# Kernel optimization log

Hardware: AMD Instinct MI355X
Metric: run time of the kernel (lower is better)

The kernel has to match this reference:

```python
import jax, jax.numpy as jnp
import numpy as np

B, S, D = 8, 1024, 576
H, HD = 9, 64
LAT = 144
FF = 1536
N_ROUTED, TOP_K = 7, 2
EPS = 1e-5
THETA = 10000.0


def setup_inputs() -> dict:
    key = jax.random.key(0)
    ks = jax.random.split(key, 20)
    sc = lambda fan_in: 1.0 / np.sqrt(fan_in)
    inp = {
        "x": jax.random.normal(ks[0], (B, S, D), jnp.float32),
        "ln1_w": jnp.ones((D,), jnp.float32),
        "ln2_w": jnp.ones((D,), jnp.float32),
        # attention projections, torch Linear layout (out, in)
        "Wqd": jax.random.normal(ks[1], (LAT, D), jnp.float32) * sc(D),
        "Wkvd": jax.random.normal(ks[2], (LAT, D), jnp.float32) * sc(D),
        "Wqu": jax.random.normal(ks[3], (D, LAT), jnp.float32) * sc(LAT),
        "Wku": jax.random.normal(ks[4], (D, LAT), jnp.float32) * sc(LAT),
        "Wvu": jax.random.normal(ks[5], (D, LAT), jnp.float32) * sc(LAT),
        "Wo": jax.random.normal(ks[6], (D, D), jnp.float32) * sc(D),
        # shared expert SwiGLU
        "sg": jax.random.normal(ks[7], (FF, D), jnp.float32) * sc(D),
        "su": jax.random.normal(ks[8], (FF, D), jnp.float32) * sc(D),
        "sd": jax.random.normal(ks[9], (D, FF), jnp.float32) * sc(FF),
        # routed experts, stacked [E, out, in]
        "rg": jax.random.normal(ks[10], (N_ROUTED, FF, D), jnp.float32) * sc(D),
        "ru": jax.random.normal(ks[11], (N_ROUTED, FF, D), jnp.float32) * sc(D),
        "rd": jax.random.normal(ks[12], (N_ROUTED, D, FF), jnp.float32) * sc(FF),
        "Wr": jax.random.normal(ks[13], (N_ROUTED, D), jnp.float32) * sc(D),
        "rb": jnp.zeros((N_ROUTED,), jnp.float32),
    }
    return inp


def _rmsnorm(x, w, eps=EPS):
    xf = x.astype(jnp.float32)
    y = xf * jax.lax.rsqrt(jnp.mean(xf * xf, axis=-1, keepdims=True) + eps)
    return y.astype(x.dtype) * w


def _rotate_half(x):
    x1, x2 = x[..., : x.shape[-1] // 2], x[..., x.shape[-1] // 2 :]
    return jnp.concatenate((-x2, x1), axis=-1)


def _rope(q, k, seq_len):
    inv_freq = 1.0 / THETA ** (jnp.arange(0, HD, 2, dtype=jnp.float32) / HD)
    freqs = jnp.arange(seq_len, dtype=jnp.float32)[:, None] * inv_freq  # [S, HD/2]
    emb = jnp.concatenate((freqs, freqs), axis=-1)  # [S, HD]
    cos = jnp.cos(emb)[None, None, :, :]
    sin = jnp.sin(emb)[None, None, :, :]
    return q * cos + _rotate_half(q) * sin, k * cos + _rotate_half(k) * sin


def _swiglu(h, Wg, Wu, Wd):
    return (jax.nn.silu(h @ Wg.T) * (h @ Wu.T)) @ Wd.T


def reference(x, ln1_w, ln2_w, Wqd, Wkvd, Wqu, Wku, Wvu, Wo,
              sg, su, sd, rg, ru, rd, Wr, rb):
    bsz, seq_len, _ = x.shape
    # ---- attention sublayer ----
    residual = x
    h = _rmsnorm(x, ln1_w)
    q_lat = h @ Wqd.T
    kv_lat = h @ Wkvd.T
    q = (q_lat @ Wqu.T).reshape(bsz, seq_len, H, HD).transpose(0, 2, 1, 3)
    k = (kv_lat @ Wku.T).reshape(bsz, seq_len, H, HD).transpose(0, 2, 1, 3)
    v = (kv_lat @ Wvu.T).reshape(bsz, seq_len, H, HD).transpose(0, 2, 1, 3)
    q, k = _rope(q, k, seq_len)
    scores = jnp.einsum("bhqd,bhkd->bhqk", q, k) / jnp.sqrt(jnp.float32(HD))
    causal = jnp.tril(jnp.ones((seq_len, seq_len), bool))
    scores = jnp.where(causal, scores, jnp.float32(-jnp.inf))
    attn = jax.nn.softmax(scores, axis=-1)
    o = jnp.einsum("bhqk,bhkd->bhqd", attn, v).transpose(0, 2, 1, 3).reshape(bsz, seq_len, D)
    x = residual + o @ Wo.T
    # ---- MoE sublayer ----
    residual = x
    h = _rmsnorm(x, ln2_w)
    shared = _swiglu(h, sg, su, sd)  # 1 shared expert
    logits = h @ Wr.T + rb
    probs = jax.nn.sigmoid(logits)
    scores_k, idx = jax.lax.top_k(probs, TOP_K)  # [B,S,K]
    scores_k = scores_k / jnp.sum(scores_k, axis=-1, keepdims=True)
    # per-token weight for each routed expert [B,S,E]
    w = jnp.sum(jax.nn.one_hot(idx, N_ROUTED, dtype=h.dtype) * scores_k[..., None], axis=-2)
    combined = jnp.zeros_like(h)
    for e in range(N_ROUTED):  # small fixed expert count
        combined = combined + w[..., e : e + 1] * _swiglu(h, rg[e], ru[e], rd[e])
    return residual + shared + combined
```

## Files before the change

kernel.cpp:

```cpp
#include <hip/hip_runtime.h>
#include <stdint.h>
#include <math.h>

#define B_    8
#define S_    1024
#define D_    576
#define H_    9
#define HD_   64
#define LAT_  144
#define FF_   1536
#define NE_   7
#define NT_   8192
#define NPAIR_ 16384
#define NACT_  24576
#define MAXT_ 200

typedef unsigned short u16;
typedef __attribute__((ext_vector_type(8))) short bf16x8;
typedef __attribute__((ext_vector_type(4))) float f32x4;
typedef __attribute__((ext_vector_type(4))) unsigned short us4;

__device__ __forceinline__ u16 f2b(float f){
  union{float f;uint32_t u;} v; v.f=f;
  uint32_t u=v.u;
  return (u16)((u + 0x7fffu + ((u>>16)&1u))>>16);
}
__device__ __forceinline__ float b2f(u16 h){
  union{uint32_t u;float f;} v; v.u=((uint32_t)h)<<16; return v.f;
}

#define MFMA16(a,b,c) __builtin_amdgcn_mfma_f32_16x16x32_bf16((a),(b),(c),0,0,0)

typedef __attribute__((address_space(1))) const unsigned char g_u8;
typedef __attribute__((address_space(3))) unsigned char s_u8;
__device__ __forceinline__ void gll16(const void* g, void* l){
  __builtin_amdgcn_global_load_lds((g_u8*)g, (s_u8*)l, 16, 0, 0);
}

struct CvtSegs {
  const float* src[6];
  u16* dst[6];
  int start4[7];
};
__global__ void k_cvt(CvtSegs cs){
  int tot = cs.start4[6];
  for(int i = blockIdx.x*blockDim.x + threadIdx.x; i < tot; i += gridDim.x*blockDim.x){
    int s=0;
    #pragma unroll
    for(int j=0;j<6;j++) if(i >= cs.start4[j+1]) s=j+1;
    int loc = i - cs.start4[s];
    float4 v = ((const float4*)cs.src[s])[loc];
    us4 o; o[0]=f2b(v.x); o[1]=f2b(v.y); o[2]=f2b(v.z); o[3]=f2b(v.w);
    ((us4*)cs.dst[s])[loc] = o;
  }
}

struct CvtSegs2 {
  const float* src[3];
  u16* dhi[3]; u16* dlo[3];
  int start4[4];
};
__global__ void k_cvt_split(CvtSegs2 cs){
  int tot = cs.start4[3];
  for(int i = blockIdx.x*blockDim.x + threadIdx.x; i < tot; i += gridDim.x*blockDim.x){
    int s=0;
    #pragma unroll
    for(int j=0;j<3;j++) if(i >= cs.start4[j+1]) s=j+1;
    int loc = i - cs.start4[s];
    float4 v = ((const float4*)cs.src[s])[loc];
    us4 oh, ol;
    float vv[4]={v.x,v.y,v.z,v.w};
    #pragma unroll
    for(int j=0;j<4;j++){ u16 hh=f2b(vv[j]); oh[j]=hh; ol[j]=f2b(vv[j]-b2f(hh)); }
    ((us4*)cs.dhi[s])[loc]=oh;
    ((us4*)cs.dlo[s])[loc]=ol;
  }
}

__global__ void k_cvt_pad_split(const float* __restrict__ Wqu, const float* __restrict__ Wku,
                                const float* __restrict__ Wvu,
                                u16* __restrict__ dhi, u16* __restrict__ dlo){
  int i = blockIdx.x*256 + threadIdx.x;
  if(i >= 3*D_*160) return;
  int z = i/(D_*160); int rem = i - z*D_*160;
  int row = rem/160, col = rem - row*160;
  const float* s = (z==0)?Wqu:((z==1)?Wku:Wvu);
  float v = (col<LAT_)? s[row*LAT_+col] : 0.f;
  u16 hh=f2b(v);
  dhi[i]=hh; dlo[i]=f2b(v-b2f(hh));
}

__global__ void k_rope_tab(float* __restrict__ cost, float* __restrict__ sint){
  int i = blockIdx.x*256+threadIdx.x; if(i>=S_*32) return;
  int s=i>>5, d=i&31;
  float pw = (float)pow(10000.0, (double)d/32.0);
  float inv = 1.0f/pw;
  float ang = (float)s*inv;
  cost[i]=cosf(ang); sint[i]=sinf(ang);
}

__global__ __launch_bounds__(64) void k_rms(const float* __restrict__ x, const float* __restrict__ w,
                      u16* __restrict__ hhi, u16* __restrict__ hlo){
  int t = blockIdx.x; int lane = threadIdx.x;
  const float* xr = x + (size_t)t*D_;
  float v[9]; float ss=0.f;
  #pragma unroll
  for(int j=0;j<9;j++){ v[j]=xr[lane+64*j]; ss += v[j]*v[j]; }
  #pragma unroll
  for(int m=1;m<64;m<<=1) ss += __shfl_xor(ss,m,64);
  float sc = 1.0f/sqrtf(ss/(float)D_ + 1e-5f);
  #pragma unroll
  for(int j=0;j<9;j++){
    float y = v[j]*sc*w[lane+64*j];
    size_t o=(size_t)t*D_+lane+64*j;
    u16 hh=f2b(y); hhi[o]=hh; hlo[o]=f2b(y-b2f(hh));
  }
}

__global__ __launch_bounds__(256) void k_rms_router(const float* __restrict__ x2, const float* __restrict__ w,
                        const float* __restrict__ Wr, const float* __restrict__ rb,
                        u16* __restrict__ hb, int* __restrict__ idx2, float* __restrict__ w2){
  int wid=threadIdx.x>>6, lane=threadIdx.x&63;
  int t = blockIdx.x*4 + wid;
  const float* xr = x2 + (size_t)t*D_;
  float v[9]; float ss=0.f;
  #pragma unroll
  for(int j=0;j<9;j++){ v[j]=xr[lane+64*j]; ss += v[j]*v[j]; }
  #pragma unroll
  for(int m=1;m<64;m<<=1) ss += __shfl_xor(ss,m,64);
  float sc = 1.0f/sqrtf(ss/(float)D_ + 1e-5f);
  float hv[9];
  #pragma unroll
  for(int j=0;j<9;j++){
    float y = v[j]*sc*w[lane+64*j];
    hv[j]=y;
    hb[(size_t)t*D_+lane+64*j]=f2b(y);
  }
  float pr[7];
  #pragma unroll
  for(int e=0;e<7;e++){
    float s=0.f;
    #pragma unroll
    for(int j=0;j<9;j++) s += hv[j]*Wr[e*D_+lane+64*j];
    #pragma unroll
    for(int mm=1;mm<64;mm<<=1) s+=__shfl_xor(s,mm,64);
    pr[e] = 1.f/(1.f+expf(-(s+rb[e])));
  }
  int e0=0; float b0=pr[0];
  #pragma unroll
  for(int e=1;e<7;e++) if(pr[e]>b0){b0=pr[e];e0=e;}
  int e1=-1; float b1=-1e30f;
  #pragma unroll
  for(int e=0;e<7;e++) if(e!=e0 && pr[e]>b1){b1=pr[e];e1=e;}
  if(lane==0){
    float s=b0+b1;
    idx2[2*t]=e0; idx2[2*t+1]=e1;
    w2[2*t]=b0/s; w2[2*t+1]=b1/s;
  }
}

template<int EPI>
__global__ __launch_bounds__(256) void k_gemm2(
    const u16* __restrict__ Ahi, const u16* __restrict__ Alo, int lda, int aofs_z,
    const u16* __restrict__ Bhi, const u16* __restrict__ Blo, int ldb, long bStrideZ,
    int N, int ksteps,
    u16* __restrict__ Chi, u16* __restrict__ Clo, int ldc,
    float* __restrict__ C32, long cStrideZ, const float* __restrict__ resid)
{
  __shared__ u16 Ahs[128*32], Als[128*32], Bhs[128*32], Bls[128*32];
  int tid=threadIdx.x, wid=tid>>6, lane=tid&63;
  int m0=blockIdx.x*128, n0=blockIdx.y*128, z=blockIdx.z;
  const u16* Abh = Ahi + ((z>0)?aofs_z:0);
  const u16* Abl = Alo + ((z>0)?aofs_z:0);
  const u16* Bbh = Bhi + (long)z*bStrideZ;
  const u16* Bbl = Blo + (long)z*bStrideZ;
  int lq=lane&15, lg=lane>>4;
  int wr=wid>>1, wc=wid&1;
  f32x4 acc[4][4]={};
  for(int kt=0;kt<ksteps;kt++){
    #pragma unroll
    for(int is=0;is<2;is++){
      int ub = is*4096 + wid*1024;
      int o = ub + lane*16;
      int row = o>>6, p=(o>>4)&3;
      int sc8 = ((p ^ ((row>>1)&3)))*8;
      long aoff = (long)(m0+row)*lda + kt*32 + sc8;
      gll16(Abh+aoff, (char*)Ahs+ub);
      gll16(Abl+aoff, (char*)Als+ub);
      int rowb = n0+row; rowb = rowb<N?rowb:(N-1);
      long boff = (long)rowb*ldb + kt*32 + sc8;
      gll16(Bbh+boff, (char*)Bhs+ub);
      gll16(Bbl+boff, (char*)Bls+ub);
    }
    __syncthreads();
    bf16x8 ah[4], al[4], bh[4], bl[4];
    #pragma unroll
    for(int m=0;m<4;m++){
      int arow=wr*64+m*16+lq;
      int co = arow*32 + ((lg ^ ((arow>>1)&3)))*8;
      ah[m]=*(const bf16x8*)&Ahs[co];
      al[m]=*(const bf16x8*)&Als[co];
    }
    #pragma unroll
    for(int n=0;n<4;n++){
      int brow=wc*64+n*16+lq;
      int co = brow*32 + ((lg ^ ((brow>>1)&3)))*8;
      bh[n]=*(const bf16x8*)&Bhs[co];
      bl[n]=*(const bf16x8*)&Bls[co];
    }
    #pragma unroll
    for(int m=0;m<4;m++)
      #pragma unroll
      for(int n=0;n<4;n++){
        acc[m][n]=MFMA16(ah[m],bh[n],acc[m][n]);
        acc[m][n]=MFMA16(ah[m],bl[n],acc[m][n]);
        acc[m][n]=MFMA16(al[m],bh[n],acc[m][n]);
      }
    __syncthreads();
  }
  #pragma unroll
  for(int m=0;m<4;m++){
    #pragma unroll
    for(int n=0;n<4;n++){
      int col = n0 + wc*64 + n*16 + lq;
      if(col<N){
        #pragma unroll
        for(int r=0;r<4;r++){
          int row = m0 + wr*64 + m*16 + lg*4 + r;
          float val = acc[m][n][r];
          if(EPI==0){
            int dc = (col<144)? col : col+16;
            u16 hh=f2b(val);
            Chi[(long)row*ldc + dc] = hh;
            Clo[(long)row*ldc + dc] = f2b(val-b2f(hh));
          } else if(EPI==1){
            (C32 + (long)z*cStrideZ)[(long)row*ldc + col] = val;
          } else {
            C32[(long)row*ldc+col] = resid[(long)row*ldc+col] + val;
          }
        }
      }
    }
  }
}

__global__ void k_ropesplit(const float* __restrict__ QR, const float* __restrict__ KR,
                            const float* __restrict__ cost, const float* __restrict__ sint,
                            u16* __restrict__ QHI, u16* __restrict__ QLO,
                            u16* __restrict__ KHI, u16* __restrict__ KLO){
  int i = blockIdx.x*256+threadIdx.x;
  if(i >= NT_*H_*32) return;
  int d = i&31; int h=(i>>5)%H_; int t = i/(H_*32);
  int s = t & (S_-1); int b = t >> 10;
  float c = cost[s*32+d], sn = sint[s*32+d];
  long qi = (long)t*D_ + h*HD_ + d;
  float q1=QR[qi], q2=QR[qi+32];
  float k1=KR[qi], k2=KR[qi+32];
  long ob = ((long)(b*H_+h)*S_ + s)*HD_ + d;
  float qa=(q1*c - q2*sn)*0.125f, qb2=(q2*c + q1*sn)*0.125f;
  float ka=k1*c - k2*sn,          kb2=k2*c + k1*sn;
  u16 hh;
  hh=f2b(qa);  QHI[ob]=hh;    QLO[ob]   =f2b(qa -b2f(hh));
  hh=f2b(qb2); QHI[ob+32]=hh; QLO[ob+32]=f2b(qb2-b2f(hh));
  hh=f2b(ka);  KHI[ob]=hh;    KLO[ob]   =f2b(ka -b2f(hh));
  hh=f2b(kb2); KHI[ob+32]=hh; KLO[ob+32]=f2b(kb2-b2f(hh));
}

__global__ __launch_bounds__(256) void k_vsplit(const float* __restrict__ VR,
                       u16* __restrict__ VHI, u16* __restrict__ VLO){
  __shared__ float ls[64][65];
  int s0 = blockIdx.x*64; int bh = blockIdx.y;
  int b = bh/H_, h = bh - b*H_;
  int tid=threadIdx.x;
  #pragma unroll
  for(int i=0;i<16;i++){
    int idx = tid + i*256;
    int si = idx>>6, dj = idx&63;
    ls[si][dj] = VR[((long)(b*S_+s0+si))*D_ + h*HD_ + dj];
  }
  __syncthreads();
  #pragma unroll
  for(int i=0;i<16;i++){
    int idx = tid + i*256;
    int di = idx>>6, sj = idx&63;
    float v = ls[sj][di];
    u16 hh = f2b(v);
    long o = ((long)bh*HD_+di)*S_ + s0+sj;
    VHI[o]=hh; VLO[o]=f2b(v-b2f(hh));
  }
}

__global__ __launch_bounds__(256) void k_attn_split(
    const u16* __restrict__ QHI, const u16* __restrict__ QLO,
    const u16* __restrict__ KHI, const u16* __restrict__ KLO,
    const u16* __restrict__ VHI, const u16* __restrict__ VLO,
    u16* __restrict__ OHI, u16* __restrict__ OLO){
  __shared__ u16 lds[2][4][64*64];
  int tid=threadIdx.x, wid=tid>>6, lane=tid&63;
  int bh=blockIdx.x; int b=bh/H_, h=bh-b*H_;
  int jb=blockIdx.y;
  int lq=lane&15, lg=lane>>4;
  int jslot=lane&7, rloc=lane>>3;

  for(int pass=0;pass<2;pass++){
    int tile = pass? (15-jb) : jb;
    int ntile = tile+1;
    int q0 = tile*64 + wid*16;
    long qoff = ((long)bh*S_ + q0+lq)*HD_;
    bf16x8 qh0 = *(const bf16x8*)(QHI+qoff+lg*8);
    bf16x8 qh1 = *(const bf16x8*)(QHI+qoff+32+lg*8);
    bf16x8 ql0 = *(const bf16x8*)(QLO+qoff+lg*8);
    bf16x8 ql1 = *(const bf16x8*)(QLO+qoff+32+lg*8);
    float m=-1e30f, l=0.f;
    f32x4 ot[4]={};
    int q_lane = q0 + lq;

    #define STAGE(bufi, kv0_) do{                                          \
      int _kv0=(kv0_);                                                     \
      _Pragma("unroll")                                                    \
      for(int c=0;c<2;c++){                                                \
        int r = wid*16 + c*8 + rloc;                                       \
        int col = 8*(jslot ^ (r&7));                                       \
        long kg = ((long)bh*S_ + _kv0 + r)*64 + col;                       \
        long vg = ((long)bh*64 + r)*S_ + _kv0 + col;                       \
        int lb = (wid*16 + c*8)*64;                                        \
        gll16(KHI+kg, &lds[bufi][0][lb]);                                  \
        gll16(KLO+kg, &lds[bufi][1][lb]);                                  \
        gll16(VHI+vg, &lds[bufi][2][lb]);                                  \
        gll16(VLO+vg, &lds[bufi][3][lb]);                                  \
      } }while(0)

    STAGE(0, 0);
    __syncthreads();
    for(int t=0;t<ntile;t++){
      if(t+1<ntile) STAGE((t+1)&1, (t+1)*64);
      int bufc = t&1;
      int kv0 = t*64;
      bool last = (t==ntile-1);
      const char* Khs=(const char*)lds[bufc][0];
      const char* Kls=(const char*)lds[bufc][1];
      const char* Vhs=(const char*)lds[bufc][2];
      const char* Vls=(const char*)lds[bufc][3];
      #pragma unroll
      for(int kvh=0;kvh<64;kvh+=32){
        float p[8];
        float tmax=-1e30f;
        #pragma unroll
        for(int sub=0;sub<2;sub++){
          int r = kvh + sub*16 + lq;
          int sw = (r&7)<<4;
          bf16x8 kh0=*(const bf16x8*)(Khs + r*128 + ((lg*16) ^ sw));
          bf16x8 kh1=*(const bf16x8*)(Khs + r*128 + ((64+lg*16) ^ sw));
          bf16x8 kl0=*(const bf16x8*)(Kls + r*128 + ((lg*16) ^ sw));
          bf16x8 kl1=*(const bf16x8*)(Kls + r*128 + ((64+lg*16) ^ sw));
          f32x4 st={0.f,0.f,0.f,0.f};
          st=MFMA16(kh0,qh0,st); st=MFMA16(kh1,qh1,st);
          st=MFMA16(kl0,qh0,st); st=MFMA16(kl1,qh1,st);
          st=MFMA16(kh0,ql0,st); st=MFMA16(kh1,ql1,st);
          #pragma unroll
          for(int r2=0;r2<4;r2++){
            int key = kv0 + kvh + sub*16 + lg*4 + r2;
            float sv = (!last || key <= q_lane)? st[r2] : -1e30f;
            p[sub*4+r2]=sv;
            tmax = fmaxf(tmax, sv);
          }
        }
        tmax = fmaxf(tmax, __shfl_xor(tmax,16,64));
        tmax = fmaxf(tmax, __shfl_xor(tmax,32,64));
        float mn = fmaxf(m, tmax);
        float sc = __expf(m - mn);
        l *= sc;
        #pragma unroll
        for(int t2=0;t2<4;t2++)
          #pragma unroll
          for(int r2=0;r2<4;r2++) ot[t2][r2]*=sc;
        float ps=0.f;
        #pragma unroll
        for(int j=0;j<8;j++){ p[j]=__expf(p[j]-mn); ps+=p[j]; }
        l+=ps; m=mn;
        bf16x8 ph, pl;
        #pragma unroll
        for(int j=0;j<8;j++){
          u16 hb2=f2b(p[j]);
          ph[j]=(short)hb2;
          pl[j]=(short)f2b(p[j]-b2f(hb2));
        }
        #pragma unroll
        for(int t2=0;t2<4;t2++){
          int d = t2*16+lq;
          int swd = (d&7)<<4;
          int b1 = (2*(kvh+4*lg)) ^ swd;
          int b2v = (2*(kvh+16+4*lg)) ^ swd;
          us4 vh0=*(const us4*)(Vhs + d*128 + b1);
          us4 vh1=*(const us4*)(Vhs + d*128 + b2v);
          us4 vl0=*(const us4*)(Vls + d*128 + b1);
          us4 vl1=*(const us4*)(Vls + d*128 + b2v);
          bf16x8 vh, vl;
          #pragma unroll
          for(int j=0;j<4;j++){
            vh[j]=(short)vh0[j]; vh[4+j]=(short)vh1[j];
            vl[j]=(short)vl0[j]; vl[4+j]=(short)vl1[j];
          }
          ot[t2]=MFMA16(vh,ph,ot[t2]);
          ot[t2]=MFMA16(vl,ph,ot[t2]);
          ot[t2]=MFMA16(vh,pl,ot[t2]);
        }
      }
      __syncthreads();
    }
    #undef STAGE
    float l1 = l + __shfl_xor(l,16,64);
    float lt = l1 + __shfl_xor(l1,32,64);
    float inv = 1.f/lt;
    long orow = ((long)b*S_ + q_lane)*D_ + h*HD_;
    #pragma unroll
    for(int t2=0;t2<4;t2++){
      us4 oh4, ol4;
      #pragma unroll
      for(int r2=0;r2<4;r2++){
        float v=ot[t2][r2]*inv;
        u16 hh=f2b(v);
        oh4[r2]=hh; ol4[r2]=f2b(v-b2f(hh));
      }
      *(us4*)(OHI + orow + t2*16 + 4*lg) = oh4;
      *(us4*)(OLO + orow + t2*16 + 4*lg) = ol4;
    }
  }
}

__global__ __launch_bounds__(256) void k_count(const int* __restrict__ idx2, int* __restrict__ counts){
  __shared__ int hist[NE_];
  int tid=threadIdx.x;
  if(tid<NE_) hist[tid]=0;
  __syncthreads();
  int i = blockIdx.x*256+tid;
  atomicAdd(&hist[idx2[i]],1);
  __syncthreads();
  if(tid<NE_) atomicAdd(&counts[tid], hist[tid]);
}

__global__ void k_offsets(const int* __restrict__ counts, int* __restrict__ ofs,
                          int* __restrict__ fill, int* __restrict__ ts){
  if(threadIdx.x==0 && blockIdx.x==0){
    int a=0;
    for(int e=0;e<NE_;e++){ ofs[e]=a; fill[e]=a; a+=counts[e]; }
    ofs[NE_]=a;
    int t=0;
    for(int e=0;e<NE_;e++){ ts[e]=t; t += (counts[e]+127)>>7; }
    ts[NE_]=t; t+=64;
    ts[NE_+1]=t;
  }
}

__global__ __launch_bounds__(256) void k_scatter2(const int* __restrict__ idx2, const float* __restrict__ w2,
                          int* __restrict__ fill, int* __restrict__ ltok,
                          float* __restrict__ lw, int* __restrict__ ppos){
  __shared__ int wcnt[4][8];
  __shared__ int wpre[4][8];
  __shared__ int base[8];
  int tid=threadIdx.x, wid=tid>>6, lane=tid&63;
  int slot = blockIdx.x*256 + wid*64 + lane;
  int id = idx2[slot];
  unsigned long long ltm = (1ull<<lane)-1ull;
  int myrank=0;
  #pragma unroll
  for(int e=0;e<7;e++){
    unsigned long long mask = __ballot(id==e);
    if(id==e) myrank = __popcll(mask & ltm);
    if(lane==0) wcnt[wid][e] = __popcll(mask);
  }
  __syncthreads();
  if(wid==0 && lane<7){
    int e=lane;
    int s0=wcnt[0][e], s1=wcnt[1][e], s2=wcnt[2][e], s3=wcnt[3][e];
    wpre[0][e]=0; wpre[1][e]=s0; wpre[2][e]=s0+s1; wpre[3][e]=s0+s1+s2;
    base[e] = atomicAdd(&fill[e], s0+s1+s2+s3);
  }
  __syncthreads();
  int pos = base[id] + wpre[wid][id] + myrank;
  ltok[pos] = slot>>1;
  lw[pos] = w2[slot];
  ppos[slot] = pos;
}

__global__ __launch_bounds__(256) void k_moe_gu(const u16* __restrict__ h2b, const u16* __restrict__ Gb,
                        const u16* __restrict__ Ub, const int* __restrict__ cnt,
                        const int* __restrict__ ofs, const int* __restrict__ ts,
                        const int* __restrict__ ltok, u16* __restrict__ act){
  int tsv[9];
  #pragma unroll
  for(int i=0;i<9;i++) tsv[i]=ts[i];
  int xt = blockIdx.x;
  if(xt >= tsv[8]) return;
  int e=0;
  #pragma unroll
  for(int i=1;i<8;i++) if(xt >= tsv[i]) e=i;
  int mt = xt - tsv[e];
  int nrows = (e<NE_)? cnt[e] : NT_;
  int base  = (e<NE_)? ofs[e] : 0;
  long arow0 = (e<NE_)? (long)base : (long)NPAIR_;
  int f0 = blockIdx.y*128;
  __shared__ u16 As[128*32], Gs[128*32], Us[128*32];
  int tid=threadIdx.x, wid=tid>>6, lane=tid&63;
  int lq=lane&15, lg=lane>>4;
  int wr=wid>>1, wc=wid&1;
  int r0 = wid*16 + (lane>>2);
  int r1 = 64 + r0;
  int sc8 = ((lane&3) ^ ((r0>>1)&3))*8;
  int ri0 = mt*128+r0; if(ri0>nrows-1) ri0=nrows-1;
  int ri1 = mt*128+r1; if(ri1>nrows-1) ri1=nrows-1;
  long tok0 = (e<NE_)? (long)ltok[base+ri0] : (long)ri0;
  long tok1 = (e<NE_)? (long)ltok[base+ri1] : (long)ri1;
  const u16* a0 = h2b + tok0*D_ + sc8;
  const u16* a1 = h2b + tok1*D_ + sc8;
  const u16* g0 = Gb + ((long)e*FF_ + f0 + r0)*D_ + sc8;
  const u16* g1 = Gb + ((long)e*FF_ + f0 + r1)*D_ + sc8;
  const u16* u0 = Ub + ((long)e*FF_ + f0 + r0)*D_ + sc8;
  const u16* u1 = Ub + ((long)e*FF_ + f0 + r1)*D_ + sc8;
  int lb0 = wid*1024 + lane*16 - (lane&3)*16 + (lane&3)*16;
  f32x4 ag_[4][4]={}, au_[4][4]={};
  for(int kt=0;kt<18;kt++){
    int ko = kt*32;
    gll16(a0+ko, (char*)As + (wid*1024 + lane*16));
    gll16(a1+ko, (char*)As + (4096 + wid*1024 + lane*16));
    gll16(g0+ko, (char*)Gs + (wid*1024 + lane*16));
    gll16(g1+ko, (char*)Gs + (4096 + wid*1024 + lane*16));
    gll16(u0+ko, (char*)Us + (wid*1024 + lane*16));
    gll16(u1+ko, (char*)Us + (4096 + wid*1024 + lane*16));
    __syncthreads();
    bf16x8 af[4], gf[4], uf[4];
    #pragma unroll
    for(int m=0;m<4;m++){
      int arow=wr*64+m*16+lq;
      af[m]=*(const bf16x8*)&As[arow*32 + ((lg ^ ((arow>>1)&3)))*8];
    }
    #pragma unroll
    for(int n=0;n<4;n++){
      int grow=wc*64+n*16+lq;
      int co = grow*32 + ((lg ^ ((grow>>1)&3)))*8;
      gf[n]=*(const bf16x8*)&Gs[co];
      uf[n]=*(const bf16x8*)&Us[co];
    }
    #pragma unroll
    for(int m=0;m<4;m++)
      #pragma unroll
      for(int n=0;n<4;n++){
        ag_[m][n]=MFMA16(af[m],gf[n],ag_[m][n]);
        au_[m][n]=MFMA16(af[m],uf[n],au_[m][n]);
      }
    __syncthreads();
  }
  (void)lb0;
  #pragma unroll
  for(int m=0;m<4;m++){
    #pragma unroll
    for(int n=0;n<4;n++){
      int f = f0 + wc*64+n*16+lq;
      #pragma unroll
      for(int r=0;r<4;r++){
        int rl = wr*64+m*16+lg*4+r;
        int ridx = mt*128+rl;
        if(ridx<nrows){
          float g=ag_[m][n][r], u=au_[m][n][r];
          float sw = g/(1.f+__expf(-g))*u;
          act[(arow0+ridx)*FF_ + f] = f2b(sw);
        }
      }
    }
  }
}

__global__ __launch_bounds__(256) void k_moe_down(const u16* __restrict__ act, const u16* __restrict__ Db,
                          const int* __restrict__ cnt, const int* __restrict__ ofs,
                          const int* __restrict__ ts, const float* __restrict__ lw,
                          u16* __restrict__ pd){
  int tsv[9];
  #pragma unroll
  for(int i=0;i<9;i++) tsv[i]=ts[i];
  int xt = blockIdx.x;
  if(xt >= tsv[8]) return;
  int e=0;
  #pragma unroll
  for(int i=1;i<8;i++) if(xt >= tsv[i]) e=i;
  int mt = xt - tsv[e];
  int nrows=(e<NE_)?cnt[e]:NT_;
  long arow0=(e<NE_)?(long)ofs[e]:(long)NPAIR_;
  int n0=blockIdx.y*128;
  __shared__ u16 As[128*32], Bs[128*32];
  int tid=threadIdx.x,wid=tid>>6,lane=tid&63;
  int lq=lane&15,lg=lane>>4;
  int wr=wid>>1,wc=wid&1;
  int r0 = wid*16 + (lane>>2);
  int r1 = 64 + r0;
  int sc8 = ((lane&3) ^ ((r0>>1)&3))*8;
  int ri0 = mt*128+r0; if(ri0>nrows-1) ri0=nrows-1;
  int ri1 = mt*128+r1; if(ri1>nrows-1) ri1=nrows-1;
  const u16* a0 = act + (arow0+ri0)*FF_ + sc8;
  const u16* a1 = act + (arow0+ri1)*FF_ + sc8;
  int rb0 = n0+r0; if(rb0>D_-1) rb0=D_-1;
  int rb1 = n0+r1; if(rb1>D_-1) rb1=D_-1;
  const u16* b0p = Db + ((long)e*D_ + rb0)*FF_ + sc8;
  const u16* b1p = Db + ((long)e*D_ + rb1)*FF_ + sc8;
  f32x4 acc[4][4]={};
  for(int kt=0;kt<48;kt++){
    int ko = kt*32;
    gll16(a0+ko, (char*)As + (wid*1024 + lane*16));
    gll16(a1+ko, (char*)As + (4096 + wid*1024 + lane*16));
    gll16(b0p+ko, (char*)Bs + (wid*1024 + lane*16));
    gll16(b1p+ko, (char*)Bs + (4096 + wid*1024 + lane*16));
    __syncthreads();
    bf16x8 af[4],bf2[4];
    #pragma unroll
    for(int m=0;m<4;m++){
      int arow=wr*64+m*16+lq;
      af[m]=*(const bf16x8*)&As[arow*32 + ((lg ^ ((arow>>1)&3)))*8];
    }
    #pragma unroll
    for(int n=0;n<4;n++){
      int brow=wc*64+n*16+lq;
      bf2[n]=*(const bf16x8*)&Bs[brow*32 + ((lg ^ ((brow>>1)&3)))*8];
    }
    #pragma unroll
    for(int m=0;m<4;m++)
      #pragma unroll
      for(int n=0;n<4;n++)
        acc[m][n]=MFMA16(af[m],bf2[n],acc[m][n]);
    __syncthreads();
  }
  #pragma unroll
  for(int m=0;m<4;m++){
    #pragma unroll
    for(int n=0;n<4;n++){
      int col=n0+wc*64+n*16+lq;
      if(col<D_){
        #pragma unroll
        for(int r=0;r<4;r++){
          int rl=wr*64+m*16+lg*4+r;
          int ridx=mt*128+rl;
          if(ridx<nrows){
            float w=1.f;
            if(e<NE_) w=lw[arow0+ridx];
            pd[(arow0+ridx)*D_ + col]=f2b(w*acc[m][n][r]);
          }
        }
      }
    }
  }
}

__global__ void k_final(const float* __restrict__ x2, const u16* __restrict__ pd,
                        const int* __restrict__ ppos, float* __restrict__ out){
  int i=blockIdx.x*256+threadIdx.x;
  int tot = NT_*(D_/4);
  if(i>=tot) return;
  int t = i/(D_/4); int c = (i - t*(D_/4))*4;
  int p0=ppos[2*t], p1=ppos[2*t+1];
  const u16* a=pd+((long)NPAIR_+t)*D_+c;
  const u16* b=pd+(long)p0*D_+c;
  const u16* d=pd+(long)p1*D_+c;
  const float* xr = x2+(long)t*D_+c;
  float* o = out+(long)t*D_+c;
  #pragma unroll
  for(int j=0;j<4;j++) o[j]=xr[j]+b2f(a[j])+b2f(b[j])+b2f(d[j]);
}

extern "C" void kernel_launch(void* const* d_in, const int* in_sizes, int n_in,
                              void* d_out, int out_size, void* d_ws, size_t ws_size,
                              hipStream_t stream){
  const float* x    =(const float*)d_in[0];
  const float* ln1  =(const float*)d_in[1];
  const float* ln2  =(const float*)d_in[2];
  const float* Wqd  =(const float*)d_in[3];
  const float* Wkvd =(const float*)d_in[4];
  const float* Wqu  =(const float*)d_in[5];
  const float* Wku  =(const float*)d_in[6];
  const float* Wvu  =(const float*)d_in[7];
  const float* Wo   =(const float*)d_in[8];
  const float* sg   =(const float*)d_in[9];
  const float* su   =(const float*)d_in[10];
  const float* sd   =(const float*)d_in[11];
  const float* rg   =(const float*)d_in[12];
  const float* ru   =(const float*)d_in[13];
  const float* rd   =(const float*)d_in[14];
  const float* Wr   =(const float*)d_in[15];
  const float* rb   =(const float*)d_in[16];
  float* out=(float*)d_out;

  char* ws=(char*)d_ws;
  size_t off=0;
  auto alloc=[&](size_t bsz){ size_t r=off; off=(off+bsz+255)&~(size_t)255; return r; };
  u16* GB   =(u16*)(ws+alloc(8L*FF_*D_*2));
  u16* UB   =(u16*)(ws+alloc(8L*FF_*D_*2));
  u16* DB   =(u16*)(ws+alloc(8L*D_*FF_*2));
  float* COS=(float*)(ws+alloc(S_*32*4));
  float* SIN=(float*)(ws+alloc(S_*32*4));
  float* X2 =(float*)(ws+alloc((long)NT_*D_*4));
  u16* H2B  =(u16*)(ws+alloc((long)NT_*D_*2));
  int* IDX2 =(int*)(ws+alloc(NT_*2*4));
  float* W2 =(float*)(ws+alloc(NT_*2*4));
  int* PPOS =(int*)(ws+alloc(NT_*2*4));
  int* CNT  =(int*)(ws+alloc(64));
  int* OFS  =(int*)(ws+alloc(64));
  int* FILL =(int*)(ws+alloc(64));
  int* TS   =(int*)(ws+alloc(64));
  int* LTOK =(int*)(ws+alloc(NPAIR_*4));
  float* LW =(float*)(ws+alloc(NPAIR_*4));
  size_t scr0 = off;
  const long NQ = (long)B_*H_*S_*HD_;
  u16* H1HI=(u16*)(ws+alloc((long)NT_*D_*2));
  u16* H1LO=(u16*)(ws+alloc((long)NT_*D_*2));
  u16* LATHI=(u16*)(ws+alloc((long)NT_*320*2));
  u16* LATLO=(u16*)(ws+alloc((long)NT_*320*2));
  float* QR =(float*)(ws+alloc((long)NT_*D_*4));
  float* KR =(float*)(ws+alloc((long)NT_*D_*4));
  float* VR =(float*)(ws+alloc((long)NT_*D_*4));
  u16* QHI =(u16*)(ws+alloc(NQ*2));
  u16* QLO =(u16*)(ws+alloc(NQ*2));
  u16* KHI =(u16*)(ws+alloc(NQ*2));
  u16* KLO =(u16*)(ws+alloc(NQ*2));
  u16* WDHI=(u16*)(ws+alloc(288L*D_*2));
  u16* WDLO=(u16*)(ws+alloc(288L*D_*2));
  u16* WUPHI=(u16*)(ws+alloc(3L*D_*160*2));
  u16* WUPLO=(u16*)(ws+alloc(3L*D_*160*2));
  u16* WOHI=(u16*)(ws+alloc((long)D_*D_*2));
  u16* WOLO=(u16*)(ws+alloc((long)D_*D_*2));
  u16* VHI = (u16*)QR;
  u16* VLO = (u16*)QR + NQ;
  u16* OHI = H1HI;
  u16* OLO = H1LO;
  off = scr0;
  u16* ACT =(u16*)(ws+alloc((long)NACT_*FF_*2));
  u16* PD  =(u16*)(ws+alloc((long)NACT_*D_*2));
  (void)ws_size;

  CvtSegs cs;
  {
    const float* ss[6]={rg,sg,ru,su,rd,sd};
    u16* dd[6]={GB, GB+7L*FF_*D_, UB, UB+7L*FF_*D_, DB, DB+7L*D_*FF_};
    long nn[6]={7L*FF_*D_,(long)FF_*D_,7L*FF_*D_,(long)FF_*D_,7L*D_*FF_,(long)D_*FF_};
    cs.start4[0]=0;
    for(int j=0;j<6;j++){ cs.src[j]=ss[j]; cs.dst[j]=dd[j]; cs.start4[j+1]=cs.start4[j]+(int)(nn[j]/4); }
  }
  k_cvt<<<2048,256,0,stream>>>(cs);
  CvtSegs2 c2;
  {
    const float* ss[3]={Wqd, Wkvd, Wo};
    u16* dh[3]={WDHI, WDHI+144L*D_, WOHI};
    u16* dl[3]={WDLO, WDLO+144L*D_, WOLO};
    long nn[3]={144L*D_, 144L*D_, (long)D_*D_};
    c2.start4[0]=0;
    for(int j=0;j<3;j++){ c2.src[j]=ss[j]; c2.dhi[j]=dh[j]; c2.dlo[j]=dl[j]; c2.start4[j+1]=c2.start4[j]+(int)(nn[j]/4); }
  }
  k_cvt_split<<<512,256,0,stream>>>(c2);
  k_cvt_pad_split<<<(3*D_*160+255)/256,256,0,stream>>>(Wqu,Wku,Wvu,WUPHI,WUPLO);
  k_rope_tab<<<(S_*32+255)/256,256,0,stream>>>(COS,SIN);

  k_rms<<<NT_,64,0,stream>>>(x, ln1, H1HI, H1LO);
  k_gemm2<0><<<dim3(64,3,1),256,0,stream>>>(H1HI,H1LO,D_,0, WDHI,WDLO,D_,0, 288,18, LATHI,LATLO,320, nullptr,0,nullptr);
  k_gemm2<1><<<dim3(64,5,3),256,0,stream>>>(LATHI,LATLO,320,160, WUPHI,WUPLO,160,(long)D_*160, D_,5, nullptr,nullptr,D_, QR,(long)NT_*D_, nullptr);
  k_ropesplit<<<(NT_*H_*32+255)/256,256,0,stream>>>(QR,KR,COS,SIN,QHI,QLO,KHI,KLO);
  k_vsplit<<<dim3(16,72),256,0,stream>>>(VR,VHI,VLO);
  k_attn_split<<<dim3(72,8),256,0,stream>>>(QHI,QLO,KHI,KLO,VHI,VLO,OHI,OLO);
  k_gemm2<2><<<dim3(64,5,1),256,0,stream>>>(OHI,OLO,D_,0, WOHI,WOLO,D_,0, D_,18, nullptr,nullptr,D_, X2,0, x);

  hipMemsetAsync(CNT,0,64,stream);
  k_rms_router<<<NT_/4,256,0,stream>>>(X2, ln2, Wr, rb, H2B, IDX2, W2);
  k_count<<<NPAIR_/256,256,0,stream>>>(IDX2,CNT);
  k_offsets<<<1,1,0,stream>>>(CNT,OFS,FILL,TS);
  k_scatter2<<<NPAIR_/256,256,0,stream>>>(IDX2,W2,FILL,LTOK,LW,PPOS);
  k_moe_gu<<<dim3(MAXT_,12),256,0,stream>>>(H2B,GB,UB,CNT,OFS,TS,LTOK,ACT);
  k_moe_down<<<dim3(MAXT_,5),256,0,stream>>>(ACT,DB,CNT,OFS,TS,LW,PD);
  k_final<<<(NT_*(D_/4)+255)/256,256,0,stream>>>(X2,PD,PPOS,out);
}
```

Before: 707.8 us.

## Double-buffer LDS in MoE GEMMs and swap grid axes for tile reuse

Both MoE GEMM kernels now keep two LDS buffers: the next K-slice is loaded asynchronously while MFMAs run on the current one, so each iteration needs one barrier instead of two. The grid axes are also swapped so that blocks sharing the same row tile (same tokens) launch next to each other, which should improve L2 reuse of the activation rows. LDS use doubles (48KB for gate-up), which may lower occupancy.

```diff
diff --git a/kernel.cpp b/kernel.cpp
--- a/kernel.cpp
+++ b/kernel.cpp
@@ -490,7 +490,7 @@
   int tsv[9];
   #pragma unroll
   for(int i=0;i<9;i++) tsv[i]=ts[i];
-  int xt = blockIdx.x;
+  int xt = blockIdx.y;
   if(xt >= tsv[8]) return;
   int e=0;
   #pragma unroll
@@ -499,13 +499,14 @@
   int nrows = (e<NE_)? cnt[e] : NT_;
   int base  = (e<NE_)? ofs[e] : 0;
   long arow0 = (e<NE_)? (long)base : (long)NPAIR_;
-  int f0 = blockIdx.y*128;
-  __shared__ u16 As[128*32], Gs[128*32], Us[128*32];
+  int f0 = blockIdx.x*128;
+  __shared__ u16 As[2][128*32], Gs[2][128*32], Us[2][128*32];
   int tid=threadIdx.x, wid=tid>>6, lane=tid&63;
   int lq=lane&15, lg=lane>>4;
   int wr=wid>>1, wc=wid&1;
   int r0 = wid*16 + (lane>>2);
   int r1 = 64 + r0;
+  int so = wid*1024 + lane*16;
   int sc8 = ((lane&3) ^ ((r0>>1)&3))*8;
   int ri0 = mt*128+r0; if(ri0>nrows-1) ri0=nrows-1;
   int ri1 = mt*128+r1; if(ri1>nrows-1) ri1=nrows-1;
@@ -517,29 +518,31 @@
   const u16* g1 = Gb + ((long)e*FF_ + f0 + r1)*D_ + sc8;
   const u16* u0 = Ub + ((long)e*FF_ + f0 + r0)*D_ + sc8;
   const u16* u1 = Ub + ((long)e*FF_ + f0 + r1)*D_ + sc8;
-  int lb0 = wid*1024 + lane*16 - (lane&3)*16 + (lane&3)*16;
+  #define STG(bi, kt_) do{ int ko=(kt_)*32;                       \
+    gll16(a0+ko, (char*)As[bi]+so);                               \
+    gll16(a1+ko, (char*)As[bi]+4096+so);                          \
+    gll16(g0+ko, (char*)Gs[bi]+so);                               \
+    gll16(g1+ko, (char*)Gs[bi]+4096+so);                          \
+    gll16(u0+ko, (char*)Us[bi]+so);                               \
+    gll16(u1+ko, (char*)Us[bi]+4096+so); }while(0)
   f32x4 ag_[4][4]={}, au_[4][4]={};
+  STG(0,0);
+  __syncthreads();
   for(int kt=0;kt<18;kt++){
-    int ko = kt*32;
-    gll16(a0+ko, (char*)As + (wid*1024 + lane*16));
-    gll16(a1+ko, (char*)As + (4096 + wid*1024 + lane*16));
-    gll16(g0+ko, (char*)Gs + (wid*1024 + lane*16));
-    gll16(g1+ko, (char*)Gs + (4096 + wid*1024 + lane*16));
-    gll16(u0+ko, (char*)Us + (wid*1024 + lane*16));
-    gll16(u1+ko, (char*)Us + (4096 + wid*1024 + lane*16));
-    __syncthreads();
+    int cur = kt&1;
+    if(kt<17) STG(cur^1, kt+1);
     bf16x8 af[4], gf[4], uf[4];
     #pragma unroll
     for(int m=0;m<4;m++){
       int arow=wr*64+m*16+lq;
-      af[m]=*(const bf16x8*)&As[arow*32 + ((lg ^ ((arow>>1)&3)))*8];
+      af[m]=*(const bf16x8*)&As[cur][arow*32 + ((lg ^ ((arow>>1)&3)))*8];
     }
     #pragma unroll
     for(int n=0;n<4;n++){
       int grow=wc*64+n*16+lq;
       int co = grow*32 + ((lg ^ ((grow>>1)&3)))*8;
-      gf[n]=*(const bf16x8*)&Gs[co];
-      uf[n]=*(const bf16x8*)&Us[co];
+      gf[n]=*(const bf16x8*)&Gs[cur][co];
+      uf[n]=*(const bf16x8*)&Us[cur][co];
     }
     #pragma unroll
     for(int m=0;m<4;m++)
@@ -550,7 +553,7 @@
       }
     __syncthreads();
   }
-  (void)lb0;
+  #undef STG
   #pragma unroll
   for(int m=0;m<4;m++){
     #pragma unroll
@@ -577,7 +580,7 @@
   int tsv[9];
   #pragma unroll
   for(int i=0;i<9;i++) tsv[i]=ts[i];
-  int xt = blockIdx.x;
+  int xt = blockIdx.y;
   if(xt >= tsv[8]) return;
   int e=0;
   #pragma unroll
@@ -585,13 +588,14 @@
   int mt = xt - tsv[e];
   int nrows=(e<NE_)?cnt[e]:NT_;
   long arow0=(e<NE_)?(long)ofs[e]:(long)NPAIR_;
-  int n0=blockIdx.y*128;
-  __shared__ u16 As[128*32], Bs[128*32];
+  int n0=blockIdx.x*128;
+  __shared__ u16 As[2][128*32], Bs[2][128*32];
   int tid=threadIdx.x,wid=tid>>6,lane=tid&63;
   int lq=lane&15,lg=lane>>4;
   int wr=wid>>1,wc=wid&1;
   int r0 = wid*16 + (lane>>2);
   int r1 = 64 + r0;
+  int so = wid*1024 + lane*16;
   int sc8 = ((lane&3) ^ ((r0>>1)&3))*8;
   int ri0 = mt*128+r0; if(ri0>nrows-1) ri0=nrows-1;
   int ri1 = mt*128+r1; if(ri1>nrows-1) ri1=nrows-1;
@@ -601,24 +605,27 @@
   int rb1 = n0+r1; if(rb1>D_-1) rb1=D_-1;
   const u16* b0p = Db + ((long)e*D_ + rb0)*FF_ + sc8;
   const u16* b1p = Db + ((long)e*D_ + rb1)*FF_ + sc8;
+  #define STG(bi, kt_) do{ int ko=(kt_)*32;                       \
+    gll16(a0+ko, (char*)As[bi]+so);                               \
+    gll16(a1+ko, (char*)As[bi]+4096+so);                          \
+    gll16(b0p+ko, (char*)Bs[bi]+so);                              \
+    gll16(b1p+ko, (char*)Bs[bi]+4096+so); }while(0)
   f32x4 acc[4][4]={};
+  STG(0,0);
+  __syncthreads();
   for(int kt=0;kt<48;kt++){
-    int ko = kt*32;
-    gll16(a0+ko, (char*)As + (wid*1024 + lane*16));
-    gll16(a1+ko, (char*)As + (4096 + wid*1024 + lane*16));
-    gll16(b0p+ko, (char*)Bs + (wid*1024 + lane*16));
-    gll16(b1p+ko, (char*)Bs + (4096 + wid*1024 + lane*16));
-    __syncthreads();
+    int cur = kt&1;
+    if(kt<47) STG(cur^1, kt+1);
     bf16x8 af[4],bf2[4];
     #pragma unroll
     for(int m=0;m<4;m++){
       int arow=wr*64+m*16+lq;
-      af[m]=*(const bf16x8*)&As[arow*32 + ((lg ^ ((arow>>1)&3)))*8];
+      af[m]=*(const bf16x8*)&As[cur][arow*32 + ((lg ^ ((arow>>1)&3)))*8];
     }
     #pragma unroll
     for(int n=0;n<4;n++){
       int brow=wc*64+n*16+lq;
-      bf2[n]=*(const bf16x8*)&Bs[brow*32 + ((lg ^ ((brow>>1)&3)))*8];
+      bf2[n]=*(const bf16x8*)&Bs[cur][brow*32 + ((lg ^ ((brow>>1)&3)))*8];
     }
     #pragma unroll
     for(int m=0;m<4;m++)
@@ -627,6 +634,7 @@
         acc[m][n]=MFMA16(af[m],bf2[n],acc[m][n]);
     __syncthreads();
   }
+  #undef STG
   #pragma unroll
   for(int m=0;m<4;m++){
     #pragma unroll
@@ -768,7 +776,7 @@
   k_count<<<NPAIR_/256,256,0,stream>>>(IDX2,CNT);
   k_offsets<<<1,1,0,stream>>>(CNT,OFS,FILL,TS);
   k_scatter2<<<NPAIR_/256,256,0,stream>>>(IDX2,W2,FILL,LTOK,LW,PPOS);
-  k_moe_gu<<<dim3(MAXT_,12),256,0,stream>>>(H2B,GB,UB,CNT,OFS,TS,LTOK,ACT);
-  k_moe_down<<<dim3(MAXT_,5),256,0,stream>>>(ACT,DB,CNT,OFS,TS,LW,PD);
+  k_moe_gu<<<dim3(12,MAXT_),256,0,stream>>>(H2B,GB,UB,CNT,OFS,TS,LTOK,ACT);
+  k_moe_down<<<dim3(5,MAXT_),256,0,stream>>>(ACT,DB,CNT,OFS,TS,LW,PD);
   k_final<<<(NT_*(D_/4)+255)/256,256,0,stream>>>(X2,PD,PPOS,out);
 }
```

Result: faster. 658.0 us (-7.0%).
